# Performance work log

Measured on AMD Instinct MI355X. Metric: run time of the kernel, lower is better.

The kernel has to match this reference:

```python
import jax, jax.numpy as jnp
import numpy as np
import math

B, S, E = 4, 2048, 1024
H, D = 16, 64

def setup_inputs() -> dict:
    key = jax.random.key(0)
    ks = jax.random.split(key, 9)
    s = 0.02
    return {
        "x":  jax.random.normal(ks[0], (B, S, E), dtype=jnp.float32),
        "Wq": jax.random.normal(ks[1], (H, E, D), dtype=jnp.float32) * s,
        "Wk": jax.random.normal(ks[2], (H, E, D), dtype=jnp.float32) * s,
        "Wv": jax.random.normal(ks[3], (H, E, D), dtype=jnp.float32) * s,
        "bq": jax.random.normal(ks[4], (H, D), dtype=jnp.float32) * s,
        "bk": jax.random.normal(ks[5], (H, D), dtype=jnp.float32) * s,
        "bv": jax.random.normal(ks[6], (H, D), dtype=jnp.float32) * s,
        "Wo": jax.random.normal(ks[7], (H * D, E), dtype=jnp.float32) * s,
        "bo": jax.random.normal(ks[8], (E,), dtype=jnp.float32) * s,
    }

def reference(x, Wq, Wk, Wv, bq, bk, bv, Wo, bo):
    # batched per-head projections: [B,S,E] x [H,E,D] -> [B,H,S,D]
    Q = jnp.einsum('bse,hed->bhsd', x, Wq) + bq[None, :, None, :]
    K = jnp.einsum('bse,hed->bhsd', x, Wk) + bk[None, :, None, :]
    V = jnp.einsum('bse,hed->bhsd', x, Wv) + bv[None, :, None, :]
    scale = 1.0 / math.sqrt(D)
    scores = jnp.einsum('bhqd,bhkd->bhqk', Q, K) * scale  # [B,H,S,S]
    causal = jnp.tril(jnp.ones((S, S), dtype=bool))
    scores = jnp.where(causal, scores, -jnp.inf)
    attn = jax.nn.softmax(scores, axis=-1)
    ctx = jnp.einsum('bhqk,bhkd->bhqd', attn, V)  # [B,H,S,D]
    # concat heads along last dim == transpose to [B,S,H,D] then reshape
    conc = ctx.transpose(0, 2, 1, 3).reshape(B, S, H * D)
    out = conc @ Wo + bo  # dropout is identity in eval
    return out
```

## Files before the change

### kernel.cpp

```cpp
#include <hip/hip_runtime.h>
#include <stdint.h>

#define Bn 4
#define Sn 2048
#define En 1024
#define Hn 16
#define Dn 64

#define QSC 0.18033688011112f

typedef unsigned short u16;
typedef short s16x8 __attribute__((ext_vector_type(8)));
typedef float f32x4 __attribute__((ext_vector_type(4)));

#define MFMA16x16x32 __builtin_amdgcn_mfma_f32_16x16x32_bf16

__device__ __forceinline__ u16 f2bf(float f) {
  union { float f; uint32_t u; } v; v.f = f;
  uint32_t u = v.u;
  u += 0x7fffu + ((u >> 16) & 1u);
  return (u16)(u >> 16);
}
__device__ __forceinline__ uint32_t f2u(float f) {
  union { float f; uint32_t u; } v; v.f = f; return v.u;
}

#define AS1 __attribute__((address_space(1)))
#define AS3 __attribute__((address_space(3)))
__device__ __forceinline__ void gload_lds16(const void* g, void* l) {
  __builtin_amdgcn_global_load_lds((const AS1 uint32_t*)g, (AS3 uint32_t*)l, 16, 0, 0);
}

__global__ void cast_x_kernel(const float4* __restrict__ in, ushort4* __restrict__ out, int n4) {
  int i = blockIdx.x * blockDim.x + threadIdx.x;
  if (i >= n4) return;
  float4 v = in[i];
  ushort4 o;
  o.x = f2bf(v.x); o.y = f2bf(v.y); o.z = f2bf(v.z); o.w = f2bf(v.w);
  out[i] = o;
}

__global__ void repack_qkv_w(const float* __restrict__ Wq, const float* __restrict__ Wk,
                             const float* __restrict__ Wv, u16* __restrict__ WallT)
{
  __shared__ float t[64][65];
  const int e0 = blockIdx.x * 64;
  const int sh = blockIdx.y;
  const int sec = sh >> 4, h = sh & 15;
  const float* W = (sec == 0) ? Wq : (sec == 1) ? Wk : Wv;
  const float* Wh = W + (size_t)h * En * Dn;
  const int tid = threadIdx.x;
  const int d = tid & 63, er = tid >> 6;
#pragma unroll
  for (int ee = 0; ee < 64; ee += 4)
    t[ee + er][d] = Wh[(size_t)(e0 + ee + er) * Dn + d];
  __syncthreads();
  const int dd = tid >> 2, eo = (tid & 3) * 16;
  u16* dst = WallT + (size_t)(sec * 1024 + h * 64 + dd) * En + e0 + eo;
#pragma unroll
  for (int i = 0; i < 16; i += 4) {
    ushort4 o;
    o.x = f2bf(t[eo + i + 0][dd]);
    o.y = f2bf(t[eo + i + 1][dd]);
    o.z = f2bf(t[eo + i + 2][dd]);
    o.w = f2bf(t[eo + i + 3][dd]);
    *(ushort4*)(dst + i) = o;
  }
}

__global__ void pack_bias(const float* __restrict__ bq, const float* __restrict__ bk,
                          const float* __restrict__ bv, float* __restrict__ biasA)
{
  int n = blockIdx.x * 256 + threadIdx.x;
  if (n >= 3 * Hn * Dn) return;
  int sec = n >> 10, rr = n & 1023;
  const float* bs = (sec == 0) ? bq : (sec == 1) ? bk : bv;
  biasA[n] = bs[rr];
}

__global__ void repack_wo(const float* __restrict__ Wo, u16* __restrict__ WoT)
{
  __shared__ float t[64][65];
  const int k0 = blockIdx.x * 64;
  const int n0 = blockIdx.y * 64;
  const int tid = threadIdx.x;
  const int c = tid & 63, r4 = tid >> 6;
#pragma unroll
  for (int rr = 0; rr < 64; rr += 4)
    t[rr + r4][c] = Wo[(size_t)(k0 + rr + r4) * En + n0 + c];
  __syncthreads();
  const int n = tid >> 2, ko = (tid & 3) * 16;
  u16* dst = WoT + (size_t)(n0 + n) * (Hn * Dn) + k0 + ko;
#pragma unroll
  for (int i = 0; i < 16; i += 4) {
    ushort4 o;
    o.x = f2bf(t[ko + i + 0][n]);
    o.y = f2bf(t[ko + i + 1][n]);
    o.z = f2bf(t[ko + i + 2][n]);
    o.w = f2bf(t[ko + i + 3][n]);
    *(ushort4*)(dst + i) = o;
  }
}

template<int MODE>
__global__ __launch_bounds__(256) void gemm_bt(
    const u16* __restrict__ A, const u16* __restrict__ Bt,
    const float* __restrict__ bias, int M, int N, int K,
    u16* __restrict__ q_out, u16* __restrict__ k_out, u16* __restrict__ v_out,
    float* __restrict__ f_out)
{
  extern __shared__ __align__(16) u16 smem[];

  const int tid  = threadIdx.x;
  const int n0   = blockIdx.x * 128;
  const int m0   = blockIdx.y * 128;
  const int w    = tid >> 6;
  const int lane = tid & 63;
  const int quad = lane >> 4;
  const int l15  = lane & 15;
  const int mbase = (w >> 1) * 64;
  const int nbase = (w & 1) * 64;
  const int swz   = (quad ^ ((l15 >> 1) & 3)) * 8;

  f32x4 acc[4][4];
#pragma unroll
  for (int i = 0; i < 4; ++i)
#pragma unroll
    for (int j = 0; j < 4; ++j)
      acc[i][j] = (f32x4){0.f, 0.f, 0.f, 0.f};

  auto stage = [&](int k0, int bf) {
    u16* lA = smem + bf * 4096;
    u16* lB = smem + 2 * 4096 + bf * 4096;
#pragma unroll
    for (int c = 0; c < 2; ++c) {
      int idx = c * 256 + tid;
      int row = idx >> 2, sl = idx & 3;
      int sg = sl ^ ((row >> 1) & 3);
      gload_lds16(A  + (size_t)(m0 + row) * K + k0 + sg * 8, &lA[idx * 8]);
      gload_lds16(Bt + (size_t)(n0 + row) * K + k0 + sg * 8, &lB[idx * 8]);
    }
  };

  stage(0, 0);
  int bf = 0;
  for (int k0 = 0; k0 < K; k0 += 32) {
    __syncthreads();
    if (k0 + 32 < K) stage(k0 + 32, bf ^ 1);
    const u16* lA = smem + bf * 4096;
    const u16* lB = smem + 2 * 4096 + bf * 4096;

    s16x8 af[4], bfr[4];
#pragma unroll
    for (int t = 0; t < 4; ++t) {
      af[t]  = *(const s16x8*)&lA[(mbase + t * 16 + l15) * 32 + swz];
      bfr[t] = *(const s16x8*)&lB[(nbase + t * 16 + l15) * 32 + swz];
    }
#pragma unroll
    for (int mt = 0; mt < 4; ++mt)
#pragma unroll
      for (int nt = 0; nt < 4; ++nt)
        acc[mt][nt] = MFMA16x16x32(af[mt], bfr[nt], acc[mt][nt], 0, 0, 0);
    bf ^= 1;
  }

  if (MODE == 0) {
    int sec = n0 >> 10;
    if (sec < 2) {
      float oscale = (sec == 0) ? QSC : 1.0f;
#pragma unroll
      for (int nt = 0; nt < 4; ++nt) {
        int col = n0 + nbase + nt * 16 + l15;
        float bv = bias[col];
        int rr = col & 1023;
        int h = rr >> 6, d = rr & 63;
        u16* dst = (sec == 0) ? q_out : k_out;
#pragma unroll
        for (int mt = 0; mt < 4; ++mt)
#pragma unroll
          for (int r = 0; r < 4; ++r) {
            int row = m0 + mbase + mt * 16 + quad * 4 + r;
            int b = row >> 11, s = row & 2047;
            dst[(((size_t)b * Hn + h) * Sn + s) * Dn + d] = f2bf((acc[mt][nt][r] + bv) * oscale);
          }
      }
    } else {
      __syncthreads();
      u16* lC = smem;
#pragma unroll
      for (int nt = 0; nt < 4; ++nt) {
        int cl = nbase + nt * 16 + l15;
        float bv = bias[n0 + cl];
#pragma unroll
        for (int mt = 0; mt < 4; ++mt)
#pragma unroll
          for (int r = 0; r < 4; ++r) {
            int rowl = mbase + mt * 16 + quad * 4 + r;
            lC[cl * 136 + rowl] = f2bf(acc[mt][nt][r] + bv);
          }
      }
      __syncthreads();
      int c  = tid >> 1, hh = tid & 1;
      int col = n0 + c;
      int h = (col >> 6) & 15, d = col & 63;
      int b = m0 >> 11;
      int s0 = (m0 & 2047) + hh * 64;
      const uint4* src = (const uint4*)&lC[c * 136 + hh * 64];
      uint4* dst = (uint4*)&v_out[(((size_t)b * Hn + h) * Dn + d) * Sn + s0];
#pragma unroll
      for (int i = 0; i < 8; ++i) dst[i] = src[i];
    }
  } else {
#pragma unroll
    for (int nt = 0; nt < 4; ++nt) {
      int col = n0 + nbase + nt * 16 + l15;
      float bv = bias[col];
#pragma unroll
      for (int mt = 0; mt < 4; ++mt)
#pragma unroll
        for (int r = 0; r < 4; ++r) {
          int row = m0 + mbase + mt * 16 + quad * 4 + r;
          f_out[(size_t)row * N + col] = acc[mt][nt][r] + bv;
        }
    }
  }
}

__global__ __launch_bounds__(256, 4) void flash_attn(
    const u16* __restrict__ Qb, const u16* __restrict__ Kb,
    const u16* __restrict__ Vt, u16* __restrict__ conc)
{
  __shared__ __align__(16) u16 lK[2][64 * 64];
  __shared__ __align__(16) u16 lV[2][64 * 64];
  __shared__ __align__(16) u16 lP[4][16 * 64];

  const int qt  = (blockIdx.x + (blockIdx.y >> 2)) & 15;
  const int bh  = blockIdx.y;
  const int b   = bh >> 4, h = bh & 15;
  const int tid = threadIdx.x;
  const int w   = tid >> 6;
  const int lane = tid & 63;
  const int quad = lane >> 4;
  const int l15  = lane & 15;
  const int q0   = qt * 128;

  const u16* Qh = Qb + (size_t)bh * Sn * Dn;
  const u16* Kh = Kb + (size_t)bh * Sn * Dn;
  const u16* Vh = Vt + (size_t)bh * Dn * Sn;

  const int Q0m[2] = { q0 + w * 16, q0 + 64 + w * 16 };

  s16x8 aq[2][2];
#pragma unroll
  for (int m = 0; m < 2; ++m)
#pragma unroll
    for (int c = 0; c < 2; ++c)
      aq[m][c] = *(const s16x8*)&Qh[(size_t)(Q0m[m] + l15) * Dn + c * 32 + quad * 8];

  s16x8 kones;
#pragma unroll
  for (int i = 0; i < 8; ++i) kones[i] = (short)0x3F80;

  f32x4 acc[2][4];
#pragma unroll
  for (int m = 0; m < 2; ++m)
#pragma unroll
    for (int i = 0; i < 4; ++i) acc[m][i] = (f32x4){0.f, 0.f, 0.f, 0.f};
  const float NEG_INF = -__builtin_inff();
  float lrow[2] = {0.f, 0.f};

  const int sw0 = (quad ^ (l15 & 7)) * 8;
  const int sw1 = ((quad + 4) ^ (l15 & 7)) * 8;
  const int l7  = l15 & 7;

  const int ntiles = 2 * qt + 2;

  auto stage = [&](int kt) {
    int bufb = kt & 1;
    int kk0 = kt * 64;
#pragma unroll
    for (int c = 0; c < 2; ++c) {
      int idx = c * 256 + tid;
      int row = idx >> 3, sl = idx & 7;
      int sg = sl ^ (row & 7);
      gload_lds16(Kh + (size_t)(kk0 + row) * Dn + sg * 8, &lK[bufb][idx * 8]);
      gload_lds16(Vh + (size_t)row * Sn + kk0 + sg * 8, &lV[bufb][idx * 8]);
    }
  };

  stage(0);
  for (int kt = 0; kt < ntiles; ++kt) {
    const int kk0 = kt * 64;
    __syncthreads();
    if (kt + 1 < ntiles) stage(kt + 1);
    const u16* cK = lK[kt & 1];
    const u16* cV = lV[kt & 1];

#pragma unroll
    for (int m = 0; m < 2; ++m) {
      const int Q0 = Q0m[m];
      if (kk0 >= Q0 + 16) continue;

      f32x4 sc[4];
#pragma unroll
      for (int ct = 0; ct < 4; ++ct) {
        s16x8 bk0 = *(const s16x8*)&cK[(ct * 16 + l15) * 64 + sw0];
        s16x8 bk1 = *(const s16x8*)&cK[(ct * 16 + l15) * 64 + sw1];
        f32x4 z = (f32x4){0.f, 0.f, 0.f, 0.f};
        z = MFMA16x16x32(bk0, aq[m][0], z, 0, 0, 0);
        z = MFMA16x16x32(bk1, aq[m][1], z, 0, 0, 0);
        sc[ct] = z;
      }

      const int qg = Q0 + l15;
      if (kk0 + 63 > Q0) {
#pragma unroll
        for (int ct = 0; ct < 4; ++ct)
#pragma unroll
          for (int r = 0; r < 4; ++r) {
            int kkg = kk0 + ct * 16 + quad * 4 + r;
            sc[ct][r] = (kkg <= qg) ? sc[ct][r] : NEG_INF;
          }
      }

#pragma unroll
      for (int ct = 0; ct < 4; ++ct)
#pragma unroll
        for (int r = 0; r < 4; ++r)
          sc[ct][r] = __builtin_amdgcn_exp2f(sc[ct][r]);

      u16* Pw = &lP[w][0];
#pragma unroll
      for (int ct = 0; ct < 4; ++ct) {
        uint32_t d0 = __builtin_amdgcn_perm(f2u(sc[ct][1]), f2u(sc[ct][0]), 0x07060302);
        uint32_t d1 = __builtin_amdgcn_perm(f2u(sc[ct][3]), f2u(sc[ct][2]), 0x07060302);
        uint2 pk; pk.x = d0; pk.y = d1;
        int seg = (ct * 2 + (quad >> 1)) ^ l7;
        *(uint2*)&Pw[l15 * 64 + seg * 8 + (quad & 1) * 4] = pk;
      }
      __builtin_amdgcn_s_waitcnt(0xc07f);

      s16x8 ap0 = *(const s16x8*)&Pw[l15 * 64 + (quad ^ l7) * 8];
      s16x8 ap1 = *(const s16x8*)&Pw[l15 * 64 + ((quad + 4) ^ l7) * 8];

      f32x4 zl = (f32x4){0.f, 0.f, 0.f, 0.f};
      zl = MFMA16x16x32(kones, ap0, zl, 0, 0, 0);
      zl = MFMA16x16x32(kones, ap1, zl, 0, 0, 0);

#pragma unroll
      for (int dt = 0; dt < 4; ++dt) {
        s16x8 bv0 = *(const s16x8*)&cV[(dt * 16 + l15) * 64 + sw0];
        s16x8 bv1 = *(const s16x8*)&cV[(dt * 16 + l15) * 64 + sw1];
        acc[m][dt] = MFMA16x16x32(bv0, ap0, acc[m][dt], 0, 0, 0);
        acc[m][dt] = MFMA16x16x32(bv1, ap1, acc[m][dt], 0, 0, 0);
      }
      lrow[m] += zl[0];
    }
  }

#pragma unroll
  for (int m = 0; m < 2; ++m) {
    float inv = 1.0f / lrow[m];
    int qg = Q0m[m] + l15;
#pragma unroll
    for (int dt = 0; dt < 4; ++dt) {
      ushort4 o;
      o.x = f2bf(acc[m][dt][0] * inv);
      o.y = f2bf(acc[m][dt][1] * inv);
      o.z = f2bf(acc[m][dt][2] * inv);
      o.w = f2bf(acc[m][dt][3] * inv);
      *(ushort4*)&conc[((size_t)b * Sn + qg) * (Hn * Dn) + h * Dn + dt * 16 + quad * 4] = o;
    }
  }
}

extern "C" void kernel_launch(void* const* d_in, const int* in_sizes, int n_in,
                              void* d_out, int out_size, void* d_ws, size_t ws_size,
                              hipStream_t stream)
{
  const float* x  = (const float*)d_in[0];
  const float* Wq = (const float*)d_in[1];
  const float* Wk = (const float*)d_in[2];
  const float* Wv = (const float*)d_in[3];
  const float* bq = (const float*)d_in[4];
  const float* bk = (const float*)d_in[5];
  const float* bv = (const float*)d_in[6];
  const float* Wo = (const float*)d_in[7];
  const float* bo = (const float*)d_in[8];
  float* out = (float*)d_out;

  char* p = (char*)d_ws;
  u16* xb    = (u16*)p; p += (size_t)Bn * Sn * En * sizeof(u16);
  u16* WallT = (u16*)p; p += (size_t)3 * Hn * Dn * En * sizeof(u16);
  u16* WoT   = (u16*)p; p += (size_t)En * Hn * Dn * sizeof(u16);
  float* biasA = (float*)p; p += (size_t)3 * Hn * Dn * sizeof(float);
  u16* Qb    = (u16*)p; p += (size_t)Bn * Hn * Sn * Dn * sizeof(u16);
  u16* Kb    = (u16*)p; p += (size_t)Bn * Hn * Sn * Dn * sizeof(u16);
  u16* Vt    = (u16*)p; p += (size_t)Bn * Hn * Dn * Sn * sizeof(u16);
  u16* conc  = (u16*)p; p += (size_t)Bn * Sn * Hn * Dn * sizeof(u16);

  int n4 = Bn * Sn * En / 4;
  cast_x_kernel<<<(n4 + 255) / 256, 256, 0, stream>>>((const float4*)x, (ushort4*)xb, n4);
  repack_qkv_w<<<dim3(En / 64, 3 * Hn), 256, 0, stream>>>(Wq, Wk, Wv, WallT);
  pack_bias<<<12, 256, 0, stream>>>(bq, bk, bv, biasA);
  repack_wo<<<dim3(Hn * Dn / 64, En / 64), 256, 0, stream>>>(Wo, WoT);

  size_t smem0 = 128 * 136 * sizeof(u16);
  gemm_bt<0><<<dim3(3 * Hn * Dn / 128, Bn * Sn / 128), 256, smem0, stream>>>(
      xb, WallT, biasA, Bn * Sn, 3 * Hn * Dn, En, Qb, Kb, Vt, nullptr);

  flash_attn<<<dim3(Sn / 128, Bn * Hn), 256, 0, stream>>>(Qb, Kb, Vt, conc);

  size_t smem1 = 4 * 4096 * sizeof(u16);
  gemm_bt<1><<<dim3(En / 128, Bn * Sn / 128), 256, smem1, stream>>>(
      conc, WoT, bo, Bn * Sn, En, Hn * Dn, nullptr, nullptr, nullptr, out);
}
```

Before: 264.9 us.

## Merge preprocessing kernels and linearize GEMM and attention grids for locality

Combines the x cast, QKV weight repack, Wo repack and bias pack into one launch that dispatches on block index, removing three kernel launches. The GEMM grids are flattened so consecutive blocks walk M first with the same N tile. The flash-attention grid is flattened so consecutive blocks cover different batch-heads, which changes the order of causal workloads across CUs and the cache sharing of weights and K/V. The changed launch orders could help or hurt L2 reuse.

```diff
diff --git a/kernel.cpp b/kernel.cpp
--- a/kernel.cpp
+++ b/kernel.cpp
@@ -31,74 +31,79 @@
   __builtin_amdgcn_global_load_lds((const AS1 uint32_t*)g, (AS3 uint32_t*)l, 16, 0, 0);
 }
 
-__global__ void cast_x_kernel(const float4* __restrict__ in, ushort4* __restrict__ out, int n4) {
-  int i = blockIdx.x * blockDim.x + threadIdx.x;
-  if (i >= n4) return;
-  float4 v = in[i];
-  ushort4 o;
-  o.x = f2bf(v.x); o.y = f2bf(v.y); o.z = f2bf(v.z); o.w = f2bf(v.w);
-  out[i] = o;
-}
-
-__global__ void repack_qkv_w(const float* __restrict__ Wq, const float* __restrict__ Wk,
-                             const float* __restrict__ Wv, u16* __restrict__ WallT)
+__global__ __launch_bounds__(256) void prep_all(
+    const float4* __restrict__ x4, ushort4* __restrict__ xb4,
+    const float* __restrict__ Wq, const float* __restrict__ Wk,
+    const float* __restrict__ Wv, u16* __restrict__ WallT,
+    const float* __restrict__ Wo, u16* __restrict__ WoT,
+    const float* __restrict__ bq, const float* __restrict__ bk,
+    const float* __restrict__ bv, float* __restrict__ biasA)
 {
   __shared__ float t[64][65];
-  const int e0 = blockIdx.x * 64;
-  const int sh = blockIdx.y;
-  const int sec = sh >> 4, h = sh & 15;
-  const float* W = (sec == 0) ? Wq : (sec == 1) ? Wk : Wv;
-  const float* Wh = W + (size_t)h * En * Dn;
   const int tid = threadIdx.x;
-  const int d = tid & 63, er = tid >> 6;
-#pragma unroll
-  for (int ee = 0; ee < 64; ee += 4)
-    t[ee + er][d] = Wh[(size_t)(e0 + ee + er) * Dn + d];
-  __syncthreads();
-  const int dd = tid >> 2, eo = (tid & 3) * 16;
-  u16* dst = WallT + (size_t)(sec * 1024 + h * 64 + dd) * En + e0 + eo;
-#pragma unroll
-  for (int i = 0; i < 16; i += 4) {
+  int blk = blockIdx.x;
+
+  if (blk < 8192) {
+    int i = blk * 256 + tid;
+    float4 v = x4[i];
     ushort4 o;
-    o.x = f2bf(t[eo + i + 0][dd]);
-    o.y = f2bf(t[eo + i + 1][dd]);
-    o.z = f2bf(t[eo + i + 2][dd]);
-    o.w = f2bf(t[eo + i + 3][dd]);
-    *(ushort4*)(dst + i) = o;
-  }
-}
-
-__global__ void pack_bias(const float* __restrict__ bq, const float* __restrict__ bk,
-                          const float* __restrict__ bv, float* __restrict__ biasA)
-{
-  int n = blockIdx.x * 256 + threadIdx.x;
-  if (n >= 3 * Hn * Dn) return;
-  int sec = n >> 10, rr = n & 1023;
-  const float* bs = (sec == 0) ? bq : (sec == 1) ? bk : bv;
-  biasA[n] = bs[rr];
-}
-
-__global__ void repack_wo(const float* __restrict__ Wo, u16* __restrict__ WoT)
-{
-  __shared__ float t[64][65];
-  const int k0 = blockIdx.x * 64;
-  const int n0 = blockIdx.y * 64;
-  const int tid = threadIdx.x;
-  const int c = tid & 63, r4 = tid >> 6;
-#pragma unroll
-  for (int rr = 0; rr < 64; rr += 4)
-    t[rr + r4][c] = Wo[(size_t)(k0 + rr + r4) * En + n0 + c];
-  __syncthreads();
-  const int n = tid >> 2, ko = (tid & 3) * 16;
-  u16* dst = WoT + (size_t)(n0 + n) * (Hn * Dn) + k0 + ko;
-#pragma unroll
-  for (int i = 0; i < 16; i += 4) {
-    ushort4 o;
-    o.x = f2bf(t[ko + i + 0][n]);
-    o.y = f2bf(t[ko + i + 1][n]);
-    o.z = f2bf(t[ko + i + 2][n]);
-    o.w = f2bf(t[ko + i + 3][n]);
-    *(ushort4*)(dst + i) = o;
+    o.x = f2bf(v.x); o.y = f2bf(v.y); o.z = f2bf(v.z); o.w = f2bf(v.w);
+    xb4[i] = o;
+    return;
+  }
+  blk -= 8192;
+  if (blk < 768) {
+    const int e0 = (blk & 15) * 64;
+    const int sh = blk >> 4;
+    const int sec = sh >> 4, h = sh & 15;
+    const float* W = (sec == 0) ? Wq : (sec == 1) ? Wk : Wv;
+    const float* Wh = W + (size_t)h * En * Dn;
+    const int d = tid & 63, er = tid >> 6;
+#pragma unroll
+    for (int ee = 0; ee < 64; ee += 4)
+      t[ee + er][d] = Wh[(size_t)(e0 + ee + er) * Dn + d];
+    __syncthreads();
+    const int dd = tid >> 2, eo = (tid & 3) * 16;
+    u16* dst = WallT + (size_t)(sec * 1024 + h * 64 + dd) * En + e0 + eo;
+#pragma unroll
+    for (int i = 0; i < 16; i += 4) {
+      ushort4 o;
+      o.x = f2bf(t[eo + i + 0][dd]);
+      o.y = f2bf(t[eo + i + 1][dd]);
+      o.z = f2bf(t[eo + i + 2][dd]);
+      o.w = f2bf(t[eo + i + 3][dd]);
+      *(ushort4*)(dst + i) = o;
+    }
+    return;
+  }
+  blk -= 768;
+  if (blk < 256) {
+    const int k0 = (blk & 15) * 64;
+    const int n0 = (blk >> 4) * 64;
+    const int c = tid & 63, r4 = tid >> 6;
+#pragma unroll
+    for (int rr = 0; rr < 64; rr += 4)
+      t[rr + r4][c] = Wo[(size_t)(k0 + rr + r4) * En + n0 + c];
+    __syncthreads();
+    const int n = tid >> 2, ko = (tid & 3) * 16;
+    u16* dst = WoT + (size_t)(n0 + n) * (Hn * Dn) + k0 + ko;
+#pragma unroll
+    for (int i = 0; i < 16; i += 4) {
+      ushort4 o;
+      o.x = f2bf(t[ko + i + 0][n]);
+      o.y = f2bf(t[ko + i + 1][n]);
+      o.z = f2bf(t[ko + i + 2][n]);
+      o.w = f2bf(t[ko + i + 3][n]);
+      *(ushort4*)(dst + i) = o;
+    }
+    return;
+  }
+  blk -= 256;
+  int n = blk * 256 + tid;
+  if (n < 3 * Hn * Dn) {
+    int sec = n >> 10, rr = n & 1023;
+    const float* bs = (sec == 0) ? bq : (sec == 1) ? bk : bv;
+    biasA[n] = bs[rr];
   }
 }
 
@@ -112,8 +117,9 @@
   extern __shared__ __align__(16) u16 smem[];
 
   const int tid  = threadIdx.x;
-  const int n0   = blockIdx.x * 128;
-  const int m0   = blockIdx.y * 128;
+  const int L    = blockIdx.x;
+  const int m0   = (L & 63) * 128;
+  const int n0   = (L >> 6) * 128;
   const int w    = tid >> 6;
   const int lane = tid & 63;
   const int quad = lane >> 4;
@@ -234,8 +240,9 @@
   __shared__ __align__(16) u16 lV[2][64 * 64];
   __shared__ __align__(16) u16 lP[4][16 * 64];
 
-  const int qt  = (blockIdx.x + (blockIdx.y >> 2)) & 15;
-  const int bh  = blockIdx.y;
+  const int L   = blockIdx.x;
+  const int bh  = L & 63;
+  const int qt  = ((L >> 6) + (bh >> 2)) & 15;
   const int b   = bh >> 4, h = bh & 15;
   const int tid = threadIdx.x;
   const int w   = tid >> 6;
@@ -399,19 +406,17 @@
   u16* Vt    = (u16*)p; p += (size_t)Bn * Hn * Dn * Sn * sizeof(u16);
   u16* conc  = (u16*)p; p += (size_t)Bn * Sn * Hn * Dn * sizeof(u16);
 
-  int n4 = Bn * Sn * En / 4;
-  cast_x_kernel<<<(n4 + 255) / 256, 256, 0, stream>>>((const float4*)x, (ushort4*)xb, n4);
-  repack_qkv_w<<<dim3(En / 64, 3 * Hn), 256, 0, stream>>>(Wq, Wk, Wv, WallT);
-  pack_bias<<<12, 256, 0, stream>>>(bq, bk, bv, biasA);
-  repack_wo<<<dim3(Hn * Dn / 64, En / 64), 256, 0, stream>>>(Wo, WoT);
+  prep_all<<<9228, 256, 0, stream>>>((const float4*)x, (ushort4*)xb,
+                                     Wq, Wk, Wv, WallT, Wo, WoT,
+                                     bq, bk, bv, biasA);
 
   size_t smem0 = 128 * 136 * sizeof(u16);
-  gemm_bt<0><<<dim3(3 * Hn * Dn / 128, Bn * Sn / 128), 256, smem0, stream>>>(
+  gemm_bt<0><<<24 * 64, 256, smem0, stream>>>(
       xb, WallT, biasA, Bn * Sn, 3 * Hn * Dn, En, Qb, Kb, Vt, nullptr);
 
-  flash_attn<<<dim3(Sn / 128, Bn * Hn), 256, 0, stream>>>(Qb, Kb, Vt, conc);
+  flash_attn<<<(Sn / 128) * Bn * Hn, 256, 0, stream>>>(Qb, Kb, Vt, conc);
 
   size_t smem1 = 4 * 4096 * sizeof(u16);
-  gemm_bt<1><<<dim3(En / 128, Bn * Sn / 128), 256, smem1, stream>>>(
+  gemm_bt<1><<<8 * 64, 256, smem1, stream>>>(
       conc, WoT, bo, Bn * Sn, En, Hn * Dn, nullptr, nullptr, nullptr, out);
 }
```

Result: faster. 250.2 us (-5.6%).
